# Performance work log

Measured on AMD Instinct MI355X. Metric: run time of the kernel, lower is better.

## Reference

```python
import jax, jax.numpy as jnp
import numpy as np

IN_FEATURES = 512
OUT_FEATURES = 1024
ALPHA = 1.0
BATCH = 8192


def setup_inputs() -> dict:
    key = jax.random.key(0)
    kx, kw = jax.random.split(key)
    x = jax.random.normal(kx, (BATCH, IN_FEATURES), dtype=jnp.float32)
    # xavier_uniform for weight of shape (out, in): limit = sqrt(6/(fan_in+fan_out))
    limit = float(np.sqrt(6.0 / (IN_FEATURES + OUT_FEATURES)))
    weight = jax.random.uniform(kw, (OUT_FEATURES, IN_FEATURES), dtype=jnp.float32,
                                minval=-limit, maxval=limit)
    return {"x": x, "weight": weight}


def reference(x, weight):
    # dist: [B, K]
    x_sq = jnp.sum(x * x, axis=1, keepdims=True)            # [B, 1]
    w_sq = jnp.sum(weight * weight, axis=1)                  # [K]
    dist = x_sq + w_sq[None, :] - 2.0 * jnp.einsum('bd,kd->bk', x, weight)
    dist = jnp.maximum(dist, 0.0)
    # Student-t kernel soft assignment
    q = (1.0 + dist / ALPHA) ** (-(ALPHA + 1.0) / 2.0)       # [B, K]
    q = q / jnp.sum(q, axis=1, keepdims=True)                # row-normalize
    return q
```

## Files before the change

### kernel.cpp

```cpp
#include <hip/hip_runtime.h>
#include <hip/hip_bf16.h>

#define BATCH 8192
#define DIM   512
#define NCL   1024
#define ROWS  32
#define BK    32
#define NCH   (DIM / BK)

typedef __bf16 bf16x8 __attribute__((ext_vector_type(8)));
typedef float  f32x4  __attribute__((ext_vector_type(4)));

__device__ __forceinline__ unsigned short f2bf(float f) {
  union { float f; unsigned u; } v; v.f = f;
  unsigned r = v.u + 0x7fffu + ((v.u >> 16) & 1u);
  return (unsigned short)(r >> 16);
}
__device__ __forceinline__ unsigned pk(float a, float b) {
  return (unsigned)f2bf(a) | ((unsigned)f2bf(b) << 16);
}

__global__ __launch_bounds__(256) void prep_w(const float* __restrict__ w,
                                              __hip_bfloat16* __restrict__ wck,
                                              float* __restrict__ wsq) {
  int k    = blockIdx.x * 4 + (threadIdx.x >> 6);
  int lane = threadIdx.x & 63;
  const float4* wrow = (const float4*)(w + (size_t)k * DIM);
  float4 a = wrow[lane * 2 + 0];
  float4 b = wrow[lane * 2 + 1];
  float s = a.x*a.x + a.y*a.y + a.z*a.z + a.w*a.w
          + b.x*b.x + b.y*b.y + b.z*b.z + b.w*b.w;
  #pragma unroll
  for (int m = 32; m >= 1; m >>= 1) s += __shfl_xor(s, m, 64);
  if (lane == 0) wsq[k] = s;
  int c = lane >> 2;
  int j = (lane & 3) * 8;
  uint4 p = { pk(a.x, a.y), pk(a.z, a.w), pk(b.x, b.y), pk(b.z, b.w) };
  *(uint4*)(wck + ((size_t)c * NCL + k) * BK + j) = p;
}

__global__ __launch_bounds__(512) void fused(const float* __restrict__ x,
                                             const __hip_bfloat16* __restrict__ wck,
                                             const float* __restrict__ wsq,
                                             float* __restrict__ out) {
  __shared__ __align__(16) __hip_bfloat16 xs2[NCH * 2 * 512];
  __shared__ float wsq_s[NCL];
  __shared__ float xsq_s[ROWS];
  __shared__ float red[ROWS][9];
  __shared__ float rowtot[ROWS];

  const int tid = threadIdx.x;
  const int r0  = blockIdx.x * ROWS;

  const int wave = tid >> 6;
  const int lane = tid & 63;
  const int m16  = lane & 15;
  const int quad = lane >> 4;
  const int col0 = wave * 128;

  bf16x8 bcur[8];
  {
    const __hip_bfloat16* wp0 = wck + (size_t)(col0 + m16) * BK + quad * 8;
    #pragma unroll
    for (int ct = 0; ct < 8; ++ct)
      bcur[ct] = *(const bf16x8*)(wp0 + ct * (16 * BK));
  }

  {
    int row = tid >> 4;
    int seg = tid & 15;
    int rt  = row >> 4, m = row & 15;
    const float4* src = (const float4*)(x + (size_t)(r0 + row) * DIM + seg * BK);
    __hip_bfloat16* dst = xs2 + (seg * 2 + rt) * 512 + m * 8;
    float ss = 0.f;
    #pragma unroll
    for (int i = 0; i < 8; ++i) {
      float4 v = src[i];
      ss += v.x*v.x + v.y*v.y + v.z*v.z + v.w*v.w;
      uint2 p = { pk(v.x, v.y), pk(v.z, v.w) };
      *(uint2*)(dst + (i >> 1) * 128 + (i & 1) * 4) = p;
    }
    ss += __shfl_xor(ss, 1, 64);
    ss += __shfl_xor(ss, 2, 64);
    ss += __shfl_xor(ss, 4, 64);
    ss += __shfl_xor(ss, 8, 64);
    if (seg == 0) xsq_s[row] = ss;
    wsq_s[tid]       = wsq[tid];
    wsq_s[tid + 512] = wsq[tid + 512];
  }

  f32x4 acc[2][8];
  #pragma unroll
  for (int rt = 0; rt < 2; ++rt)
    #pragma unroll
    for (int ct = 0; ct < 8; ++ct)
      acc[rt][ct] = (f32x4){0.f, 0.f, 0.f, 0.f};

  __syncthreads();

  bf16x8 a0 = *(const bf16x8*)(xs2 + 0 * 512 + lane * 8);
  bf16x8 a1 = *(const bf16x8*)(xs2 + 1 * 512 + lane * 8);

  #pragma unroll
  for (int c = 0; c < NCH; ++c) {
    bf16x8 bnx[8], na0, na1;
    if (c + 1 < NCH) {
      const __hip_bfloat16* wp = wck + ((size_t)(c + 1) * NCL + col0 + m16) * BK + quad * 8;
      #pragma unroll
      for (int ct = 0; ct < 8; ++ct)
        bnx[ct] = *(const bf16x8*)(wp + ct * (16 * BK));
      na0 = *(const bf16x8*)(xs2 + ((c + 1) * 2 + 0) * 512 + lane * 8);
      na1 = *(const bf16x8*)(xs2 + ((c + 1) * 2 + 1) * 512 + lane * 8);
    }
    #pragma unroll
    for (int ct = 0; ct < 8; ++ct) {
      acc[0][ct] = __builtin_amdgcn_mfma_f32_16x16x32_bf16(a0, bcur[ct], acc[0][ct], 0, 0, 0);
      acc[1][ct] = __builtin_amdgcn_mfma_f32_16x16x32_bf16(a1, bcur[ct], acc[1][ct], 0, 0, 0);
    }
    if (c + 1 < NCH) {
      #pragma unroll
      for (int ct = 0; ct < 8; ++ct) bcur[ct] = bnx[ct];
      a0 = na0; a1 = na1;
    }
  }

  float part[2][4];
  #pragma unroll
  for (int rt = 0; rt < 2; ++rt)
    #pragma unroll
    for (int i = 0; i < 4; ++i) part[rt][i] = 0.f;

  #pragma unroll
  for (int rt = 0; rt < 2; ++rt) {
    float xq[4];
    #pragma unroll
    for (int i = 0; i < 4; ++i) xq[i] = xsq_s[rt * 16 + quad * 4 + i];
    #pragma unroll
    for (int ct = 0; ct < 8; ++ct) {
      float wq = wsq_s[col0 + ct * 16 + m16];
      #pragma unroll
      for (int i = 0; i < 4; ++i) {
        float dist = fmaxf(xq[i] + wq - 2.f * acc[rt][ct][i], 0.f);
        float qu = 1.f / (1.f + dist);
        acc[rt][ct][i] = qu;
        part[rt][i] += qu;
      }
    }
  }
  #pragma unroll
  for (int rt = 0; rt < 2; ++rt)
    #pragma unroll
    for (int i = 0; i < 4; ++i) {
      float s = part[rt][i];
      s += __shfl_xor(s, 1, 64);
      s += __shfl_xor(s, 2, 64);
      s += __shfl_xor(s, 4, 64);
      s += __shfl_xor(s, 8, 64);
      part[rt][i] = s;
    }
  if (m16 == 0) {
    #pragma unroll
    for (int rt = 0; rt < 2; ++rt)
      #pragma unroll
      for (int i = 0; i < 4; ++i)
        red[rt * 16 + quad * 4 + i][wave] = part[rt][i];
  }
  __syncthreads();
  if (tid < ROWS) {
    float t = 0.f;
    #pragma unroll
    for (int w2 = 0; w2 < 8; ++w2) t += red[tid][w2];
    rowtot[tid] = 1.f / t;
  }
  __syncthreads();
  #pragma unroll
  for (int rt = 0; rt < 2; ++rt) {
    #pragma unroll
    for (int i = 0; i < 4; ++i) {
      int r = rt * 16 + quad * 4 + i;
      float inv = rowtot[r];
      float* orow = out + (size_t)(r0 + r) * NCL + col0 + m16;
      #pragma unroll
      for (int ct = 0; ct < 8; ++ct)
        __builtin_nontemporal_store(acc[rt][ct][i] * inv, orow + ct * 16);
    }
  }
}

extern "C" void kernel_launch(void* const* d_in, const int* in_sizes, int n_in,
                              void* d_out, int out_size, void* d_ws, size_t ws_size,
                              hipStream_t stream) {
  const float* x = (const float*)d_in[0];
  const float* w = (const float*)d_in[1];
  __hip_bfloat16* wck = (__hip_bfloat16*)d_ws;
  float* wsq = (float*)((char*)d_ws + (size_t)NCH * NCL * BK * 2);
  float* out = (float*)d_out;

  hipLaunchKernelGGL(prep_w, dim3(NCL / 4), dim3(256), 0, stream, w, wck, wsq);
  hipLaunchKernelGGL(fused, dim3(BATCH / ROWS), dim3(512), 0, stream, x, wck, wsq, out);
}
```

Before: 110.0 us.

## Split fused block across 16 waves with 64 columns each

Doubles the workgroup to 1024 threads so each wave covers 64 cluster columns instead of 128. This halves per-wave accumulators and B-fragment registers and adds more waves for latency hiding. The x staging is remapped: each thread converts 16 floats, and row norms are reduced through a new shared partial array, which costs an extra barrier. The output stores switch from nontemporal to plain stores, which changes cache behaviour on the large output write.

After: 97.68 us. -11.2%, faster.

```diff
diff --git a/kernel.cpp b/kernel.cpp
--- a/kernel.cpp
+++ b/kernel.cpp
@@ -7,6 +7,7 @@
 #define ROWS  32
 #define BK    32
 #define NCH   (DIM / BK)
+#define NWAVE 16
 
 typedef __bf16 bf16x8 __attribute__((ext_vector_type(8)));
 typedef float  f32x4  __attribute__((ext_vector_type(4)));
@@ -39,14 +40,15 @@
   *(uint4*)(wck + ((size_t)c * NCL + k) * BK + j) = p;
 }
 
-__global__ __launch_bounds__(512) void fused(const float* __restrict__ x,
-                                             const __hip_bfloat16* __restrict__ wck,
-                                             const float* __restrict__ wsq,
-                                             float* __restrict__ out) {
+__global__ __launch_bounds__(1024, 4) void fused(const float* __restrict__ x,
+                                                 const __hip_bfloat16* __restrict__ wck,
+                                                 const float* __restrict__ wsq,
+                                                 float* __restrict__ out) {
   __shared__ __align__(16) __hip_bfloat16 xs2[NCH * 2 * 512];
   __shared__ float wsq_s[NCL];
+  __shared__ float xqp[NWAVE][33];
   __shared__ float xsq_s[ROWS];
-  __shared__ float red[ROWS][9];
+  __shared__ float red[ROWS][NWAVE + 1];
   __shared__ float rowtot[ROWS];
 
   const int tid = threadIdx.x;
@@ -56,46 +58,51 @@
   const int lane = tid & 63;
   const int m16  = lane & 15;
   const int quad = lane >> 4;
-  const int col0 = wave * 128;
-
-  bf16x8 bcur[8];
+  const int col0 = wave * 64;
+
+  bf16x8 bcur[4];
   {
     const __hip_bfloat16* wp0 = wck + (size_t)(col0 + m16) * BK + quad * 8;
     #pragma unroll
-    for (int ct = 0; ct < 8; ++ct)
+    for (int ct = 0; ct < 4; ++ct)
       bcur[ct] = *(const bf16x8*)(wp0 + ct * (16 * BK));
   }
 
   {
-    int row = tid >> 4;
-    int seg = tid & 15;
-    int rt  = row >> 4, m = row & 15;
-    const float4* src = (const float4*)(x + (size_t)(r0 + row) * DIM + seg * BK);
-    __hip_bfloat16* dst = xs2 + (seg * 2 + rt) * 512 + m * 8;
-    float ss = 0.f;
-    #pragma unroll
-    for (int i = 0; i < 8; ++i) {
-      float4 v = src[i];
-      ss += v.x*v.x + v.y*v.y + v.z*v.z + v.w*v.w;
-      uint2 p = { pk(v.x, v.y), pk(v.z, v.w) };
-      *(uint2*)(dst + (i >> 1) * 128 + (i & 1) * 4) = p;
-    }
-    ss += __shfl_xor(ss, 1, 64);
-    ss += __shfl_xor(ss, 2, 64);
-    ss += __shfl_xor(ss, 4, 64);
-    ss += __shfl_xor(ss, 8, 64);
-    if (seg == 0) xsq_s[row] = ss;
-    wsq_s[tid]       = wsq[tid];
-    wsq_s[tid + 512] = wsq[tid + 512];
-  }
-
-  f32x4 acc[2][8];
+    int row = tid & 31;
+    int seg = tid >> 5;
+    int c = seg >> 1, h = seg & 1;
+    int rt = row >> 4, m = row & 15;
+    const float4* src = (const float4*)(x + (size_t)(r0 + row) * DIM + seg * 16);
+    float4 v0 = src[0], v1 = src[1], v2 = src[2], v3 = src[3];
+    float ss = v0.x*v0.x + v0.y*v0.y + v0.z*v0.z + v0.w*v0.w
+             + v1.x*v1.x + v1.y*v1.y + v1.z*v1.z + v1.w*v1.w
+             + v2.x*v2.x + v2.y*v2.y + v2.z*v2.z + v2.w*v2.w
+             + v3.x*v3.x + v3.y*v3.y + v3.z*v3.z + v3.w*v3.w;
+    __hip_bfloat16* base = xs2 + (c * 2 + rt) * 512 + m * 8;
+    uint4 p0 = { pk(v0.x, v0.y), pk(v0.z, v0.w), pk(v1.x, v1.y), pk(v1.z, v1.w) };
+    uint4 p1 = { pk(v2.x, v2.y), pk(v2.z, v2.w), pk(v3.x, v3.y), pk(v3.z, v3.w) };
+    *(uint4*)(base + (h * 2 + 0) * 128) = p0;
+    *(uint4*)(base + (h * 2 + 1) * 128) = p1;
+    ss += __shfl_xor(ss, 32, 64);
+    if (lane < 32) xqp[wave][row] = ss;
+    wsq_s[tid] = wsq[tid];
+  }
+
+  f32x4 acc[2][4];
   #pragma unroll
   for (int rt = 0; rt < 2; ++rt)
     #pragma unroll
-    for (int ct = 0; ct < 8; ++ct)
+    for (int ct = 0; ct < 4; ++ct)
       acc[rt][ct] = (f32x4){0.f, 0.f, 0.f, 0.f};
 
+  __syncthreads();
+  if (tid < ROWS) {
+    float t = 0.f;
+    #pragma unroll
+    for (int w2 = 0; w2 < NWAVE; ++w2) t += xqp[w2][tid];
+    xsq_s[tid] = t;
+  }
   __syncthreads();
 
   bf16x8 a0 = *(const bf16x8*)(xs2 + 0 * 512 + lane * 8);
@@ -103,23 +110,23 @@
 
   #pragma unroll
   for (int c = 0; c < NCH; ++c) {
-    bf16x8 bnx[8], na0, na1;
+    bf16x8 bnx[4], na0, na1;
     if (c + 1 < NCH) {
       const __hip_bfloat16* wp = wck + ((size_t)(c + 1) * NCL + col0 + m16) * BK + quad * 8;
       #pragma unroll
-      for (int ct = 0; ct < 8; ++ct)
+      for (int ct = 0; ct < 4; ++ct)
         bnx[ct] = *(const bf16x8*)(wp + ct * (16 * BK));
       na0 = *(const bf16x8*)(xs2 + ((c + 1) * 2 + 0) * 512 + lane * 8);
       na1 = *(const bf16x8*)(xs2 + ((c + 1) * 2 + 1) * 512 + lane * 8);
     }
     #pragma unroll
-    for (int ct = 0; ct < 8; ++ct) {
+    for (int ct = 0; ct < 4; ++ct) {
       acc[0][ct] = __builtin_amdgcn_mfma_f32_16x16x32_bf16(a0, bcur[ct], acc[0][ct], 0, 0, 0);
       acc[1][ct] = __builtin_amdgcn_mfma_f32_16x16x32_bf16(a1, bcur[ct], acc[1][ct], 0, 0, 0);
     }
     if (c + 1 < NCH) {
       #pragma unroll
-      for (int ct = 0; ct < 8; ++ct) bcur[ct] = bnx[ct];
+      for (int ct = 0; ct < 4; ++ct) bcur[ct] = bnx[ct];
       a0 = na0; a1 = na1;
     }
   }
@@ -136,7 +143,7 @@
     #pragma unroll
     for (int i = 0; i < 4; ++i) xq[i] = xsq_s[rt * 16 + quad * 4 + i];
     #pragma unroll
-    for (int ct = 0; ct < 8; ++ct) {
+    for (int ct = 0; ct < 4; ++ct) {
       float wq = wsq_s[col0 + ct * 16 + m16];
       #pragma unroll
       for (int i = 0; i < 4; ++i) {
@@ -169,7 +176,7 @@
   if (tid < ROWS) {
     float t = 0.f;
     #pragma unroll
-    for (int w2 = 0; w2 < 8; ++w2) t += red[tid][w2];
+    for (int w2 = 0; w2 < NWAVE; ++w2) t += red[tid][w2];
     rowtot[tid] = 1.f / t;
   }
   __syncthreads();
@@ -181,8 +188,8 @@
       float inv = rowtot[r];
       float* orow = out + (size_t)(r0 + r) * NCL + col0 + m16;
       #pragma unroll
-      for (int ct = 0; ct < 8; ++ct)
-        __builtin_nontemporal_store(acc[rt][ct][i] * inv, orow + ct * 16);
+      for (int ct = 0; ct < 4; ++ct)
+        orow[ct * 16] = acc[rt][ct][i] * inv;
     }
   }
 }
@@ -197,5 +204,5 @@
   float* out = (float*)d_out;
 
   hipLaunchKernelGGL(prep_w, dim3(NCL / 4), dim3(256), 0, stream, w, wck, wsq);
-  hipLaunchKernelGGL(fused, dim3(BATCH / ROWS), dim3(512), 0, stream, x, wck, wsq, out);
-}
+  hipLaunchKernelGGL(fused, dim3(BATCH / ROWS), dim3(1024), 0, stream, x, wck, wsq, out);
+}
```

## Halve rows per block to 16 and raise occupancy with launch bounds

Applied to the files above, without the earlier changes.

Each block now handles 16 rows instead of 32, so there are twice as many blocks, and each wave holds half as many accumulators. A minimum of 4 blocks per CU is requested through launch bounds to allow more resident waves. The x staging loop is rewritten to use 32 threads per row with wider LDS stores, and the output stores switch from nontemporal to regular stores. In exchange, each bf16 W fragment loaded from global memory now feeds only one MFMA instead of two, which doubles total W traffic through the cache.

Result: faster. 105.1 us (-4.4%).

```diff
diff --git a/kernel.cpp b/kernel.cpp
--- a/kernel.cpp
+++ b/kernel.cpp
@@ -4,9 +4,10 @@
 #define BATCH 8192
 #define DIM   512
 #define NCL   1024
-#define ROWS  32
+#define ROWS  16
 #define BK    32
 #define NCH   (DIM / BK)
+#define NWAVE 8
 
 typedef __bf16 bf16x8 __attribute__((ext_vector_type(8)));
 typedef float  f32x4  __attribute__((ext_vector_type(4)));
@@ -39,14 +40,14 @@
   *(uint4*)(wck + ((size_t)c * NCL + k) * BK + j) = p;
 }
 
-__global__ __launch_bounds__(512) void fused(const float* __restrict__ x,
-                                             const __hip_bfloat16* __restrict__ wck,
-                                             const float* __restrict__ wsq,
-                                             float* __restrict__ out) {
-  __shared__ __align__(16) __hip_bfloat16 xs2[NCH * 2 * 512];
+__global__ __launch_bounds__(512, 4) void fused(const float* __restrict__ x,
+                                                const __hip_bfloat16* __restrict__ wck,
+                                                const float* __restrict__ wsq,
+                                                float* __restrict__ out) {
+  __shared__ __align__(16) __hip_bfloat16 xs2[NCH * 512];
   __shared__ float wsq_s[NCL];
   __shared__ float xsq_s[ROWS];
-  __shared__ float red[ROWS][9];
+  __shared__ float red[ROWS][NWAVE + 1];
   __shared__ float rowtot[ROWS];
 
   const int tid = threadIdx.x;
@@ -67,123 +68,104 @@
   }
 
   {
-    int row = tid >> 4;
-    int seg = tid & 15;
-    int rt  = row >> 4, m = row & 15;
-    const float4* src = (const float4*)(x + (size_t)(r0 + row) * DIM + seg * BK);
-    __hip_bfloat16* dst = xs2 + (seg * 2 + rt) * 512 + m * 8;
-    float ss = 0.f;
-    #pragma unroll
-    for (int i = 0; i < 8; ++i) {
-      float4 v = src[i];
-      ss += v.x*v.x + v.y*v.y + v.z*v.z + v.w*v.w;
-      uint2 p = { pk(v.x, v.y), pk(v.z, v.w) };
-      *(uint2*)(dst + (i >> 1) * 128 + (i & 1) * 4) = p;
-    }
+    int row = tid >> 5;
+    int seg = tid & 31;
+    int c = seg >> 1, h = seg & 1;
+    const f32x4* src = (const f32x4*)(x + (size_t)(r0 + row) * DIM + seg * 16);
+    f32x4 v0 = src[0], v1 = src[1], v2 = src[2], v3 = src[3];
+    float ss = v0.x*v0.x + v0.y*v0.y + v0.z*v0.z + v0.w*v0.w
+             + v1.x*v1.x + v1.y*v1.y + v1.z*v1.z + v1.w*v1.w
+             + v2.x*v2.x + v2.y*v2.y + v2.z*v2.z + v2.w*v2.w
+             + v3.x*v3.x + v3.y*v3.y + v3.z*v3.z + v3.w*v3.w;
+    __hip_bfloat16* base = xs2 + c * 512 + row * 8;
+    uint4 p0 = { pk(v0.x, v0.y), pk(v0.z, v0.w), pk(v1.x, v1.y), pk(v1.z, v1.w) };
+    uint4 p1 = { pk(v2.x, v2.y), pk(v2.z, v2.w), pk(v3.x, v3.y), pk(v3.z, v3.w) };
+    *(uint4*)(base + (h * 2 + 0) * 128) = p0;
+    *(uint4*)(base + (h * 2 + 1) * 128) = p1;
     ss += __shfl_xor(ss, 1, 64);
     ss += __shfl_xor(ss, 2, 64);
     ss += __shfl_xor(ss, 4, 64);
     ss += __shfl_xor(ss, 8, 64);
-    if (seg == 0) xsq_s[row] = ss;
+    ss += __shfl_xor(ss, 16, 64);
+    if ((lane & 31) == 0) xsq_s[row] = ss;
     wsq_s[tid]       = wsq[tid];
     wsq_s[tid + 512] = wsq[tid + 512];
   }
 
-  f32x4 acc[2][8];
+  f32x4 acc[8];
   #pragma unroll
-  for (int rt = 0; rt < 2; ++rt)
-    #pragma unroll
-    for (int ct = 0; ct < 8; ++ct)
-      acc[rt][ct] = (f32x4){0.f, 0.f, 0.f, 0.f};
+  for (int ct = 0; ct < 8; ++ct)
+    acc[ct] = (f32x4){0.f, 0.f, 0.f, 0.f};
 
   __syncthreads();
 
-  bf16x8 a0 = *(const bf16x8*)(xs2 + 0 * 512 + lane * 8);
-  bf16x8 a1 = *(const bf16x8*)(xs2 + 1 * 512 + lane * 8);
+  bf16x8 a_cur = *(const bf16x8*)(xs2 + lane * 8);
 
   #pragma unroll
   for (int c = 0; c < NCH; ++c) {
-    bf16x8 bnx[8], na0, na1;
+    bf16x8 bnx[8], a_nxt;
     if (c + 1 < NCH) {
       const __hip_bfloat16* wp = wck + ((size_t)(c + 1) * NCL + col0 + m16) * BK + quad * 8;
       #pragma unroll
       for (int ct = 0; ct < 8; ++ct)
         bnx[ct] = *(const bf16x8*)(wp + ct * (16 * BK));
-      na0 = *(const bf16x8*)(xs2 + ((c + 1) * 2 + 0) * 512 + lane * 8);
-      na1 = *(const bf16x8*)(xs2 + ((c + 1) * 2 + 1) * 512 + lane * 8);
+      a_nxt = *(const bf16x8*)(xs2 + (c + 1) * 512 + lane * 8);
     }
     #pragma unroll
-    for (int ct = 0; ct < 8; ++ct) {
-      acc[0][ct] = __builtin_amdgcn_mfma_f32_16x16x32_bf16(a0, bcur[ct], acc[0][ct], 0, 0, 0);
-      acc[1][ct] = __builtin_amdgcn_mfma_f32_16x16x32_bf16(a1, bcur[ct], acc[1][ct], 0, 0, 0);
-    }
+    for (int ct = 0; ct < 8; ++ct)
+      acc[ct] = __builtin_amdgcn_mfma_f32_16x16x32_bf16(a_cur, bcur[ct], acc[ct], 0, 0, 0);
     if (c + 1 < NCH) {
+      a_cur = a_nxt;
       #pragma unroll
       for (int ct = 0; ct < 8; ++ct) bcur[ct] = bnx[ct];
-      a0 = na0; a1 = na1;
     }
   }
 
-  float part[2][4];
+  float part[4] = {0.f, 0.f, 0.f, 0.f};
+  float xq[4];
   #pragma unroll
-  for (int rt = 0; rt < 2; ++rt)
+  for (int i = 0; i < 4; ++i) xq[i] = xsq_s[quad * 4 + i];
+  #pragma unroll
+  for (int ct = 0; ct < 8; ++ct) {
+    float wq = wsq_s[col0 + ct * 16 + m16];
     #pragma unroll
-    for (int i = 0; i < 4; ++i) part[rt][i] = 0.f;
-
-  #pragma unroll
-  for (int rt = 0; rt < 2; ++rt) {
-    float xq[4];
-    #pragma unroll
-    for (int i = 0; i < 4; ++i) xq[i] = xsq_s[rt * 16 + quad * 4 + i];
-    #pragma unroll
-    for (int ct = 0; ct < 8; ++ct) {
-      float wq = wsq_s[col0 + ct * 16 + m16];
-      #pragma unroll
-      for (int i = 0; i < 4; ++i) {
-        float dist = fmaxf(xq[i] + wq - 2.f * acc[rt][ct][i], 0.f);
-        float qu = 1.f / (1.f + dist);
-        acc[rt][ct][i] = qu;
-        part[rt][i] += qu;
-      }
+    for (int i = 0; i < 4; ++i) {
+      float dist = fmaxf(xq[i] + wq - 2.f * acc[ct][i], 0.f);
+      float qu = 1.f / (1.f + dist);
+      acc[ct][i] = qu;
+      part[i] += qu;
     }
   }
   #pragma unroll
-  for (int rt = 0; rt < 2; ++rt)
-    #pragma unroll
-    for (int i = 0; i < 4; ++i) {
-      float s = part[rt][i];
-      s += __shfl_xor(s, 1, 64);
-      s += __shfl_xor(s, 2, 64);
-      s += __shfl_xor(s, 4, 64);
-      s += __shfl_xor(s, 8, 64);
-      part[rt][i] = s;
-    }
+  for (int i = 0; i < 4; ++i) {
+    float s = part[i];
+    s += __shfl_xor(s, 1, 64);
+    s += __shfl_xor(s, 2, 64);
+    s += __shfl_xor(s, 4, 64);
+    s += __shfl_xor(s, 8, 64);
+    part[i] = s;
+  }
   if (m16 == 0) {
     #pragma unroll
-    for (int rt = 0; rt < 2; ++rt)
-      #pragma unroll
-      for (int i = 0; i < 4; ++i)
-        red[rt * 16 + quad * 4 + i][wave] = part[rt][i];
+    for (int i = 0; i < 4; ++i)
+      red[quad * 4 + i][wave] = part[i];
   }
   __syncthreads();
   if (tid < ROWS) {
     float t = 0.f;
     #pragma unroll
-    for (int w2 = 0; w2 < 8; ++w2) t += red[tid][w2];
+    for (int w2 = 0; w2 < NWAVE; ++w2) t += red[tid][w2];
     rowtot[tid] = 1.f / t;
   }
   __syncthreads();
   #pragma unroll
-  for (int rt = 0; rt < 2; ++rt) {
+  for (int i = 0; i < 4; ++i) {
+    int r = quad * 4 + i;
+    float inv = rowtot[r];
+    float* orow = out + (size_t)(r0 + r) * NCL + col0 + m16;
     #pragma unroll
-    for (int i = 0; i < 4; ++i) {
-      int r = rt * 16 + quad * 4 + i;
-      float inv = rowtot[r];
-      float* orow = out + (size_t)(r0 + r) * NCL + col0 + m16;
-      #pragma unroll
-      for (int ct = 0; ct < 8; ++ct)
-        __builtin_nontemporal_store(acc[rt][ct][i] * inv, orow + ct * 16);
-    }
+    for (int ct = 0; ct < 8; ++ct)
+      orow[ct * 16] = acc[ct][i] * inv;
   }
 }
 
```
